# Kernel optimization log

Hardware: AMD Instinct MI355X
Metric: run time of the kernel (lower is better)

## Reference

```python
import jax, jax.numpy as jnp
import numpy as np

EPS = 1e-12  # matches torch F.normalize default eps

def l2norm(t):
    n = jnp.linalg.norm(t, axis=-1, keepdims=True)
    return t / jnp.maximum(n, EPS)

def rotate_half(x):
    # '... (j d) -> ... j d' with j=2: split into two halves, return cat(-x2, x1)
    x1, x2 = jnp.split(x, 2, axis=-1)
    return jnp.concatenate((-x2, x1), axis=-1)

def rotary_freqs(seq_len, dim):
    inv_freq = 1.0 / (10000.0 ** (jnp.arange(0, dim, 2, dtype=jnp.float32) / dim))
    seq = jnp.arange(seq_len, dtype=jnp.float32)
    freqs = seq[:, None] * inv_freq[None, :]          # [n, d/2]
    emb = jnp.concatenate((freqs, freqs), axis=-1)    # [n, d]
    return emb[None, None]                            # [1, 1, n, d]

def apply_rotary_pos_emb(t, freqs):
    # rot_dim == dim_head here, so the pass-through slice is empty
    return t * jnp.cos(freqs) + rotate_half(t) * jnp.sin(freqs)

def setup_inputs() -> dict:
    key = jax.random.key(0)
    kq, kk, kv = jax.random.split(key, 3)
    b, h, n, d = 2, 16, 2048, 64
    q = jax.random.normal(kq, (b, h, n, d), dtype=jnp.float32)
    k = jax.random.normal(kk, (b, h, n, d), dtype=jnp.float32)
    v = jax.random.normal(kv, (b, h, n, d), dtype=jnp.float32)
    q_scale = jnp.ones((d,), dtype=jnp.float32)
    k_scale = jnp.ones((d,), dtype=jnp.float32)
    return {"q": q, "k": k, "v": v, "q_scale": q_scale, "k_scale": k_scale}

def reference(q, k, v, q_scale, k_scale):
    b, h, n, d = q.shape
    # QK RMSNorm (l2 normalize + learned per-dim scale)
    q = l2norm(q) * q_scale
    k = l2norm(k) * k_scale
    # rotary position embedding (always applied in the source module)
    freqs = rotary_freqs(n, d)
    q = apply_rotary_pos_emb(q, freqs)
    k = apply_rotary_pos_emb(k, freqs)
    # attention: explicit scores -> softmax -> values
    scale = d ** -0.5
    sim = jnp.einsum('bhid,bhjd->bhij', q, k) * scale
    attn = jax.nn.softmax(sim, axis=-1)
    out = jnp.einsum('bhij,bhjd->bhid', attn, v)
    # 'b h n d -> b n (h d)'
    return out.transpose(0, 2, 1, 3).reshape(b, n, h * d)
```

## Files before the change

### kernel.cpp

```cpp
#include <hip/hip_runtime.h>
#include <math.h>

#define BH   32
#define NSEQ 2048
#define DH   64
#define NH   16
#define LOG2E 1.44269504088896f

typedef _Float16 f16x8 __attribute__((ext_vector_type(8)));
typedef __fp16   fp16x2 __attribute__((ext_vector_type(2)));
typedef float    f32x16v __attribute__((ext_vector_type(16)));

#if __has_builtin(__builtin_amdgcn_exp2f)
#define EXP2F(x) __builtin_amdgcn_exp2f(x)
#else
#define EXP2F(x) exp2f(x)
#endif

static __device__ __forceinline__ unsigned packh_rne(float a, float b) {
    union { _Float16 h[2]; unsigned u; } x;
    x.h[0] = (_Float16)a; x.h[1] = (_Float16)b;
    return x.u;
}
static __device__ __forceinline__ unsigned pkrtz(float a, float b) {
    fp16x2 r = __builtin_amdgcn_cvt_pkrtz(a, b);
    return __builtin_bit_cast(unsigned, r);
}
#if __has_builtin(__builtin_amdgcn_perm)
#define PERM(a, b, s) __builtin_amdgcn_perm((a), (b), (s))
#else
static __device__ __forceinline__ unsigned PERM(unsigned a, unsigned b, unsigned s) {
    if (s == 0x05040100u) return (b & 0xffffu) | (a << 16);
    return (b >> 16) | (a & 0xffff0000u);
}
#endif

static __device__ __forceinline__ void unpack_pairs(const unsigned* rr, uint4& lo, uint4& hi) {
    lo.x = PERM(rr[1], rr[0], 0x05040100u);  hi.x = PERM(rr[1], rr[0], 0x07060302u);
    lo.y = PERM(rr[3], rr[2], 0x05040100u);  hi.y = PERM(rr[3], rr[2], 0x07060302u);
    lo.z = PERM(rr[5], rr[4], 0x05040100u);  hi.z = PERM(rr[5], rr[4], 0x07060302u);
    lo.w = PERM(rr[7], rr[6], 0x05040100u);  hi.w = PERM(rr[7], rr[6], 0x07060302u);
}

__global__ void freq_kernel(float2* __restrict__ tab) {
    int idx = blockIdx.x * 256 + threadIdx.x;
    int pos = idx >> 5, p = idx & 31;
    float inv_freq = powf(10000.0f, -(float)p / 32.0f);
    float sn, cs;
    sincosf((float)pos * inv_freq, &sn, &cs);
    tab[idx] = make_float2(cs, sn);
}

__global__ void prep_kernel(const float* __restrict__ in, const float* __restrict__ scale,
                            const float2* __restrict__ tab,
                            unsigned* __restrict__ out, float smul) {
    const int w = threadIdx.x >> 6, lane = threadIdx.x & 63;
    const int c = lane & 31, hfr = lane >> 5;
    const int row = blockIdx.x * 8 + w * 2 + hfr;
    const size_t base = (size_t)row * DH;
    float2 x2 = *(const float2*)(in + base + 2 * c);
    float ss = x2.x * x2.x + x2.y * x2.y;
    #pragma unroll
    for (int off = 16; off > 0; off >>= 1) ss += __shfl_xor(ss, off);
    float inv = 1.0f / fmaxf(sqrtf(ss), 1e-12f);
    float2 sc = *(const float2*)(scale + 2 * c);
    float t0 = x2.x * inv * sc.x;
    float t1 = x2.y * inv * sc.y;
    float p0 = __shfl_xor(t0, 16);
    float p1 = __shfl_xor(t1, 16);
    float r0 = (c < 16) ? -p0 : p0;
    float r1 = (c < 16) ? -p1 : p1;
    int pos = row & (NSEQ - 1);
    float4 cc = *(const float4*)((const float*)(tab + pos * 32) + ((2 * c) & 31) * 2);
    float o0 = (t0 * cc.x + r0 * cc.y) * smul;
    float o1 = (t1 * cc.z + r1 * cc.w) * smul;
    out[row * 32 + c] = packh_rne(o0, o1);
}

__global__ void vpack_kernel(const float* __restrict__ v, unsigned* __restrict__ vt2) {
    const int kt = blockIdx.x, bh = blockIdx.y;
    const int t = threadIdx.x;
    const int r = t & 63, ch = t >> 6;
    const float* src = v + ((size_t)bh * NSEQ + kt * 64 + r) * DH + ch * 16;
    float4 a = *(const float4*)(src + 0);
    float4 b = *(const float4*)(src + 4);
    float4 c2 = *(const float4*)(src + 8);
    float4 d2 = *(const float4*)(src + 12);
    unsigned* dst = vt2 + ((size_t)bh * 32 + ch * 8) * NSEQ + kt * 64 + r;
    dst[0 * NSEQ] = packh_rne(a.x, a.y);
    dst[1 * NSEQ] = packh_rne(a.z, a.w);
    dst[2 * NSEQ] = packh_rne(b.x, b.y);
    dst[3 * NSEQ] = packh_rne(b.z, b.w);
    dst[4 * NSEQ] = packh_rne(c2.x, c2.y);
    dst[5 * NSEQ] = packh_rne(c2.z, c2.w);
    dst[6 * NSEQ] = packh_rne(d2.x, d2.y);
    dst[7 * NSEQ] = packh_rne(d2.z, d2.w);
}

__global__ __launch_bounds__(256, 2) void attn_kernel(
    const unsigned* __restrict__ qh, const unsigned* __restrict__ kh,
    const unsigned* __restrict__ vt2, float* __restrict__ out) {

    __shared__ _Float16 Ks[2][64 * 72];
    __shared__ _Float16 Vs[2][64 * 72];

    const int bh = blockIdx.y, qb = blockIdx.x;
    const int tid = threadIdx.x;
    const int w = tid >> 6, lane = tid & 63;
    const int c = lane & 31, hf = lane >> 5;

    const _Float16* qbase = (const _Float16*)qh + ((size_t)bh * NSEQ + qb * 128) * DH;
    const _Float16* kbase = (const _Float16*)kh + (size_t)bh * NSEQ * DH;
    const unsigned* vbase = vt2 + (size_t)bh * 32 * NSEQ;

    const int sdp = tid >> 3, skc = tid & 7;

    #pragma unroll
    for (int i = 0; i < 2; ++i) {
        int chunk = tid + 256 * i;
        int r = chunk >> 3, sg = chunk & 7;
        *(uint4*)&Ks[0][r * 72 + sg * 8] = *(const uint4*)(kbase + r * 64 + sg * 8);
    }
    {
        const unsigned* vsrc = vbase + (size_t)sdp * NSEQ + skc * 8;
        unsigned rr[8];
        #pragma unroll
        for (int j = 0; j < 8; ++j) rr[j] = vsrc[j];
        uint4 lo, hi;
        unpack_pairs(rr, lo, hi);
        *(uint4*)&Vs[0][(2 * sdp) * 72 + skc * 8]     = lo;
        *(uint4*)&Vs[0][(2 * sdp + 1) * 72 + skc * 8] = hi;
    }

    f16x8 qf[4];
    #pragma unroll
    for (int ks = 0; ks < 4; ++ks)
        qf[ks] = *(const f16x8*)(qbase + (w * 32 + c) * 64 + ks * 16 + hf * 8);

    f32x16v o[2];
    #pragma unroll
    for (int mt = 0; mt < 2; ++mt)
        #pragma unroll
        for (int r = 0; r < 16; ++r) o[mt][r] = 0.f;
    float lpart = 0.f;

    __syncthreads();

    for (int jt = 0; jt < 32; ++jt) {
        const int cur = jt & 1;
        uint4 kpre[2];
        unsigned vpre[8];
        if (jt + 1 < 32) {
            const _Float16* kn = kbase + (size_t)(jt + 1) * 64 * DH;
            #pragma unroll
            for (int i = 0; i < 2; ++i) {
                int chunk = tid + 256 * i;
                int r = chunk >> 3, sg = chunk & 7;
                kpre[i] = *(const uint4*)(kn + r * 64 + sg * 8);
            }
            const unsigned* vsrc = vbase + (size_t)sdp * NSEQ + (jt + 1) * 64 + skc * 8;
            #pragma unroll
            for (int j = 0; j < 8; ++j) vpre[j] = vsrc[j];
        }

        f32x16v s[2];
        #pragma unroll
        for (int mt = 0; mt < 2; ++mt)
            #pragma unroll
            for (int r = 0; r < 16; ++r) s[mt][r] = 0.f;
        #pragma unroll
        for (int ks = 0; ks < 4; ++ks) {
            f16x8 ka0 = *(const f16x8*)&Ks[cur][c * 72 + ks * 16 + hf * 8];
            f16x8 ka1 = *(const f16x8*)&Ks[cur][(32 + c) * 72 + ks * 16 + hf * 8];
            s[0] = __builtin_amdgcn_mfma_f32_32x32x16_f16(ka0, qf[ks], s[0], 0, 0, 0);
            s[1] = __builtin_amdgcn_mfma_f32_32x32x16_f16(ka1, qf[ks], s[1], 0, 0, 0);
        }

        #pragma unroll
        for (int mt = 0; mt < 2; ++mt)
            #pragma unroll
            for (int r = 0; r < 16; ++r) {
                float pv = EXP2F(s[mt][r]);
                s[mt][r] = pv;
                lpart += pv;
            }

        #pragma unroll
        for (int mt = 0; mt < 2; ++mt) {
            #pragma unroll
            for (int kk = 0; kk < 2; ++kk) {
                unsigned P01 = pkrtz(s[mt][kk * 8 + 0], s[mt][kk * 8 + 1]);
                unsigned P23 = pkrtz(s[mt][kk * 8 + 2], s[mt][kk * 8 + 3]);
                unsigned P45 = pkrtz(s[mt][kk * 8 + 4], s[mt][kk * 8 + 5]);
                unsigned P67 = pkrtz(s[mt][kk * 8 + 6], s[mt][kk * 8 + 7]);
                unsigned x01 = (unsigned)__shfl_xor((int)P01, 32);
                unsigned x23 = (unsigned)__shfl_xor((int)P23, 32);
                unsigned x45 = (unsigned)__shfl_xor((int)P45, 32);
                unsigned x67 = (unsigned)__shfl_xor((int)P67, 32);
                union { unsigned u[4]; f16x8 v; } B;
                B.u[0] = hf ? x45 : P01;
                B.u[1] = hf ? x67 : P23;
                B.u[2] = hf ? P45 : x01;
                B.u[3] = hf ? P67 : x23;
                const int kc = mt * 2 + kk;
                f16x8 va0 = *(const f16x8*)&Vs[cur][c * 72 + kc * 16 + hf * 8];
                f16x8 va1 = *(const f16x8*)&Vs[cur][(32 + c) * 72 + kc * 16 + hf * 8];
                o[0] = __builtin_amdgcn_mfma_f32_32x32x16_f16(va0, B.v, o[0], 0, 0, 0);
                o[1] = __builtin_amdgcn_mfma_f32_32x32x16_f16(va1, B.v, o[1], 0, 0, 0);
            }
        }

        if (jt + 1 < 32) {
            #pragma unroll
            for (int i = 0; i < 2; ++i) {
                int chunk = tid + 256 * i;
                int r = chunk >> 3, sg = chunk & 7;
                *(uint4*)&Ks[1 - cur][r * 72 + sg * 8] = kpre[i];
            }
            uint4 lo, hi;
            unpack_pairs(vpre, lo, hi);
            *(uint4*)&Vs[1 - cur][(2 * sdp) * 72 + skc * 8]     = lo;
            *(uint4*)&Vs[1 - cur][(2 * sdp + 1) * 72 + skc * 8] = hi;
        }
        __syncthreads();
    }

    float ltot = lpart + __shfl_xor(lpart, 32);
    float invl = 1.0f / ltot;
    const int b = bh >> 4, h = bh & 15;
    const int pos = qb * 128 + w * 32 + c;
    float* obase = out + ((size_t)b * NSEQ + pos) * (NH * DH) + h * DH;
    #pragma unroll
    for (int mt = 0; mt < 2; ++mt)
        #pragma unroll
        for (int g = 0; g < 4; ++g) {
            float4 r4 = make_float4(o[mt][g * 4 + 0] * invl, o[mt][g * 4 + 1] * invl,
                                    o[mt][g * 4 + 2] * invl, o[mt][g * 4 + 3] * invl);
            *(float4*)(obase + mt * 32 + g * 8 + hf * 4) = r4;
        }
}

extern "C" void kernel_launch(void* const* d_in, const int* in_sizes, int n_in,
                              void* d_out, int out_size, void* d_ws, size_t ws_size,
                              hipStream_t stream) {
    const float* q  = (const float*)d_in[0];
    const float* k  = (const float*)d_in[1];
    const float* v  = (const float*)d_in[2];
    const float* qs = (const float*)d_in[3];
    const float* ks = (const float*)d_in[4];
    float* outp = (float*)d_out;

    unsigned* qh  = (unsigned*)d_ws;
    unsigned* kh  = qh + (size_t)BH * NSEQ * 32;
    unsigned* vt2 = kh + (size_t)BH * NSEQ * 32;
    float2*   tab = (float2*)(vt2 + (size_t)BH * NSEQ * 32);

    freq_kernel<<<256, 256, 0, stream>>>(tab);
    prep_kernel<<<BH * NSEQ / 8, 256, 0, stream>>>(q, qs, tab, qh, 0.125f * LOG2E);
    prep_kernel<<<BH * NSEQ / 8, 256, 0, stream>>>(k, ks, tab, kh, 1.0f);
    vpack_kernel<<<dim3(NSEQ / 64, BH), 256, 0, stream>>>(v, vt2);
    attn_kernel<<<dim3(NSEQ / 128, BH), 256, 0, stream>>>(qh, kh, vt2, outp);
}
```

Baseline: 154.1 us.

## Fuse prep kernels and split attention key range across two warp groups

Merges the frequency table, Q/K normalization+rotary and V packing into a single prep kernel, with sin/cos computed per block in shared memory. The attention kernel now uses 512 threads, where two groups of four waves each handle half of the key sequence with 32-key tiles, and partial outputs and row sums are combined through shared memory at the end. This is meant to cut launch overhead and raise per-block parallelism and occupancy. The cost is an extra shared-memory reduction, recomputed sincos per block, and smaller tiles with more barriers.

```diff
diff --git a/kernel.cpp b/kernel.cpp
--- a/kernel.cpp
+++ b/kernel.cpp
@@ -35,107 +35,109 @@
 }
 #endif
 
-static __device__ __forceinline__ void unpack_pairs(const unsigned* rr, uint4& lo, uint4& hi) {
-    lo.x = PERM(rr[1], rr[0], 0x05040100u);  hi.x = PERM(rr[1], rr[0], 0x07060302u);
-    lo.y = PERM(rr[3], rr[2], 0x05040100u);  hi.y = PERM(rr[3], rr[2], 0x07060302u);
-    lo.z = PERM(rr[5], rr[4], 0x05040100u);  hi.z = PERM(rr[5], rr[4], 0x07060302u);
-    lo.w = PERM(rr[7], rr[6], 0x05040100u);  hi.w = PERM(rr[7], rr[6], 0x07060302u);
-}
-
-__global__ void freq_kernel(float2* __restrict__ tab) {
-    int idx = blockIdx.x * 256 + threadIdx.x;
-    int pos = idx >> 5, p = idx & 31;
-    float inv_freq = powf(10000.0f, -(float)p / 32.0f);
-    float sn, cs;
-    sincosf((float)pos * inv_freq, &sn, &cs);
-    tab[idx] = make_float2(cs, sn);
-}
-
-__global__ void prep_kernel(const float* __restrict__ in, const float* __restrict__ scale,
-                            const float2* __restrict__ tab,
-                            unsigned* __restrict__ out, float smul) {
-    const int w = threadIdx.x >> 6, lane = threadIdx.x & 63;
-    const int c = lane & 31, hfr = lane >> 5;
-    const int row = blockIdx.x * 8 + w * 2 + hfr;
-    const size_t base = (size_t)row * DH;
-    float2 x2 = *(const float2*)(in + base + 2 * c);
-    float ss = x2.x * x2.x + x2.y * x2.y;
-    #pragma unroll
-    for (int off = 16; off > 0; off >>= 1) ss += __shfl_xor(ss, off);
-    float inv = 1.0f / fmaxf(sqrtf(ss), 1e-12f);
-    float2 sc = *(const float2*)(scale + 2 * c);
-    float t0 = x2.x * inv * sc.x;
-    float t1 = x2.y * inv * sc.y;
-    float p0 = __shfl_xor(t0, 16);
-    float p1 = __shfl_xor(t1, 16);
-    float r0 = (c < 16) ? -p0 : p0;
-    float r1 = (c < 16) ? -p1 : p1;
-    int pos = row & (NSEQ - 1);
-    float4 cc = *(const float4*)((const float*)(tab + pos * 32) + ((2 * c) & 31) * 2);
-    float o0 = (t0 * cc.x + r0 * cc.y) * smul;
-    float o1 = (t1 * cc.z + r1 * cc.w) * smul;
-    out[row * 32 + c] = packh_rne(o0, o1);
-}
-
-__global__ void vpack_kernel(const float* __restrict__ v, unsigned* __restrict__ vt2) {
-    const int kt = blockIdx.x, bh = blockIdx.y;
+__global__ __launch_bounds__(256) void prep_all(
+    const float* __restrict__ q, const float* __restrict__ k, const float* __restrict__ v,
+    const float* __restrict__ qs, const float* __restrict__ ksc,
+    unsigned* __restrict__ qh, unsigned* __restrict__ kh, unsigned* __restrict__ vt2) {
+    const int bid = blockIdx.x;
     const int t = threadIdx.x;
-    const int r = t & 63, ch = t >> 6;
-    const float* src = v + ((size_t)bh * NSEQ + kt * 64 + r) * DH + ch * 16;
-    float4 a = *(const float4*)(src + 0);
-    float4 b = *(const float4*)(src + 4);
-    float4 c2 = *(const float4*)(src + 8);
-    float4 d2 = *(const float4*)(src + 12);
-    unsigned* dst = vt2 + ((size_t)bh * 32 + ch * 8) * NSEQ + kt * 64 + r;
-    dst[0 * NSEQ] = packh_rne(a.x, a.y);
-    dst[1 * NSEQ] = packh_rne(a.z, a.w);
-    dst[2 * NSEQ] = packh_rne(b.x, b.y);
-    dst[3 * NSEQ] = packh_rne(b.z, b.w);
-    dst[4 * NSEQ] = packh_rne(c2.x, c2.y);
-    dst[5 * NSEQ] = packh_rne(c2.z, c2.w);
-    dst[6 * NSEQ] = packh_rne(d2.x, d2.y);
-    dst[7 * NSEQ] = packh_rne(d2.z, d2.w);
-}
-
-__global__ __launch_bounds__(256, 2) void attn_kernel(
-    const unsigned* __restrict__ qh, const unsigned* __restrict__ kh,
+    if (bid < 16384) {
+        const bool isq = bid < 8192;
+        const float* in = isq ? q : k;
+        const float* sc = isq ? qs : ksc;
+        unsigned* outp  = isq ? qh : kh;
+        const float smul = isq ? 0.125f * LOG2E : 1.0f;
+        const int sb = bid & 8191;
+        __shared__ float2 tab[8][32];
+        {
+            int pr = t >> 5, p = t & 31;
+            int pos = (sb * 8 + pr) & (NSEQ - 1);
+            float infr = exp2f(-(float)p * (13.287712379549449f / 32.0f));
+            float sn, cs;
+            sincosf((float)pos * infr, &sn, &cs);
+            tab[pr][p] = make_float2(cs, sn);
+        }
+        __syncthreads();
+        const int w = t >> 6, lane = t & 63;
+        const int c = lane & 31, hfr = lane >> 5;
+        const int rl = w * 2 + hfr;
+        const int row = sb * 8 + rl;
+        float2 x2 = *(const float2*)(in + (size_t)row * DH + 2 * c);
+        float ss = x2.x * x2.x + x2.y * x2.y;
+        #pragma unroll
+        for (int off = 16; off > 0; off >>= 1) ss += __shfl_xor(ss, off);
+        float inv = 1.0f / fmaxf(sqrtf(ss), 1e-12f);
+        float2 s2 = *(const float2*)(sc + 2 * c);
+        float t0 = x2.x * inv * s2.x;
+        float t1 = x2.y * inv * s2.y;
+        float p0 = __shfl_xor(t0, 16);
+        float p1 = __shfl_xor(t1, 16);
+        float r0 = (c < 16) ? -p0 : p0;
+        float r1 = (c < 16) ? -p1 : p1;
+        float4 cc = *(const float4*)&tab[rl][(2 * c) & 31];
+        float o0 = (t0 * cc.x + r0 * cc.y) * smul;
+        float o1 = (t1 * cc.z + r1 * cc.w) * smul;
+        outp[row * 32 + c] = packh_rne(o0, o1);
+    } else {
+        const int sb = bid - 16384;
+        const int kt = sb & 31, bh = sb >> 5;
+        const int r = t & 63, ch = t >> 6;
+        const float* src = v + ((size_t)bh * NSEQ + kt * 64 + r) * DH + ch * 16;
+        float4 a = *(const float4*)(src + 0);
+        float4 b = *(const float4*)(src + 4);
+        float4 c2 = *(const float4*)(src + 8);
+        float4 d2 = *(const float4*)(src + 12);
+        unsigned* dst = vt2 + ((size_t)bh * 32 + ch * 8) * NSEQ + kt * 64 + r;
+        dst[0 * NSEQ] = packh_rne(a.x, a.y);
+        dst[1 * NSEQ] = packh_rne(a.z, a.w);
+        dst[2 * NSEQ] = packh_rne(b.x, b.y);
+        dst[3 * NSEQ] = packh_rne(b.z, b.w);
+        dst[4 * NSEQ] = packh_rne(c2.x, c2.y);
+        dst[5 * NSEQ] = packh_rne(c2.z, c2.w);
+        dst[6 * NSEQ] = packh_rne(d2.x, d2.y);
+        dst[7 * NSEQ] = packh_rne(d2.z, d2.w);
+    }
+}
+
+__global__ __launch_bounds__(512, 4) void attn_kernel(
+    const unsigned* __restrict__ qh, const unsigned* __restrict__ khg,
     const unsigned* __restrict__ vt2, float* __restrict__ out) {
 
-    __shared__ _Float16 Ks[2][64 * 72];
-    __shared__ _Float16 Vs[2][64 * 72];
+    __shared__ __align__(16) unsigned char SMEM[36864];
+    _Float16* KsB = (_Float16*)SMEM;
+    _Float16* VsB = (_Float16*)(SMEM + 18432);
+    float* Red = (float*)SMEM;
 
     const int bh = blockIdx.y, qb = blockIdx.x;
     const int tid = threadIdx.x;
-    const int w = tid >> 6, lane = tid & 63;
+    const int kh = tid >> 8;
+    const int ltid = tid & 255;
+    const int w = tid >> 6, wq = w & 3;
+    const int lane = tid & 63;
     const int c = lane & 31, hf = lane >> 5;
 
     const _Float16* qbase = (const _Float16*)qh + ((size_t)bh * NSEQ + qb * 128) * DH;
-    const _Float16* kbase = (const _Float16*)kh + (size_t)bh * NSEQ * DH;
-    const unsigned* vbase = vt2 + (size_t)bh * 32 * NSEQ;
-
-    const int sdp = tid >> 3, skc = tid & 7;
-
-    #pragma unroll
-    for (int i = 0; i < 2; ++i) {
-        int chunk = tid + 256 * i;
-        int r = chunk >> 3, sg = chunk & 7;
-        *(uint4*)&Ks[0][r * 72 + sg * 8] = *(const uint4*)(kbase + r * 64 + sg * 8);
-    }
+    const _Float16* kbase = (const _Float16*)khg + ((size_t)bh * NSEQ + kh * 1024) * DH;
+    const unsigned* vbase = vt2 + (size_t)bh * 32 * NSEQ + kh * 1024;
+
+    const int skr = ltid >> 3, ssg = ltid & 7;
+    const int sdp = ltid >> 3, skq = (ltid & 7) * 4;
+
     {
-        const unsigned* vsrc = vbase + (size_t)sdp * NSEQ + skc * 8;
-        unsigned rr[8];
-        #pragma unroll
-        for (int j = 0; j < 8; ++j) rr[j] = vsrc[j];
-        uint4 lo, hi;
-        unpack_pairs(rr, lo, hi);
-        *(uint4*)&Vs[0][(2 * sdp) * 72 + skc * 8]     = lo;
-        *(uint4*)&Vs[0][(2 * sdp + 1) * 72 + skc * 8] = hi;
+        *(uint4*)&KsB[(kh * 2 + 0) * 2304 + skr * 72 + ssg * 8] =
+            *(const uint4*)(kbase + skr * DH + ssg * 8);
+        uint4 vr = *(const uint4*)(vbase + (size_t)sdp * NSEQ + skq);
+        uint2 lo, hi;
+        lo.x = PERM(vr.y, vr.x, 0x05040100u); hi.x = PERM(vr.y, vr.x, 0x07060302u);
+        lo.y = PERM(vr.w, vr.z, 0x05040100u); hi.y = PERM(vr.w, vr.z, 0x07060302u);
+        *(uint2*)&VsB[(kh * 2 + 0) * 2304 + (2 * sdp) * 36 + skq]     = lo;
+        *(uint2*)&VsB[(kh * 2 + 0) * 2304 + (2 * sdp + 1) * 36 + skq] = hi;
     }
 
     f16x8 qf[4];
     #pragma unroll
     for (int ks = 0; ks < 4; ++ks)
-        qf[ks] = *(const f16x8*)(qbase + (w * 32 + c) * 64 + ks * 16 + hf * 8);
+        qf[ks] = *(const f16x8*)(qbase + (wq * 32 + c) * DH + ks * 16 + hf * 8);
 
     f32x16v o[2];
     #pragma unroll
@@ -148,96 +150,96 @@
 
     for (int jt = 0; jt < 32; ++jt) {
         const int cur = jt & 1;
-        uint4 kpre[2];
-        unsigned vpre[8];
+        const _Float16* KsCur = KsB + (kh * 2 + cur) * 2304;
+        const _Float16* VsCur = VsB + (kh * 2 + cur) * 2304;
+
+        uint4 kpre, vpre;
         if (jt + 1 < 32) {
-            const _Float16* kn = kbase + (size_t)(jt + 1) * 64 * DH;
-            #pragma unroll
-            for (int i = 0; i < 2; ++i) {
-                int chunk = tid + 256 * i;
-                int r = chunk >> 3, sg = chunk & 7;
-                kpre[i] = *(const uint4*)(kn + r * 64 + sg * 8);
-            }
-            const unsigned* vsrc = vbase + (size_t)sdp * NSEQ + (jt + 1) * 64 + skc * 8;
-            #pragma unroll
-            for (int j = 0; j < 8; ++j) vpre[j] = vsrc[j];
-        }
-
-        f32x16v s[2];
+            kpre = *(const uint4*)(kbase + (size_t)(jt + 1) * 32 * DH + skr * DH + ssg * 8);
+            vpre = *(const uint4*)(vbase + (size_t)sdp * NSEQ + (jt + 1) * 32 + skq);
+        }
+
+        f32x16v s;
+        #pragma unroll
+        for (int r = 0; r < 16; ++r) s[r] = 0.f;
+        #pragma unroll
+        for (int ks = 0; ks < 4; ++ks) {
+            f16x8 ka = *(const f16x8*)&KsCur[c * 72 + ks * 16 + hf * 8];
+            s = __builtin_amdgcn_mfma_f32_32x32x16_f16(ka, qf[ks], s, 0, 0, 0);
+        }
+
+        #pragma unroll
+        for (int r = 0; r < 16; ++r) {
+            float pv = EXP2F(s[r]);
+            s[r] = pv;
+            lpart += pv;
+        }
+
+        #pragma unroll
+        for (int kk = 0; kk < 2; ++kk) {
+            unsigned P01 = pkrtz(s[kk * 8 + 0], s[kk * 8 + 1]);
+            unsigned P23 = pkrtz(s[kk * 8 + 2], s[kk * 8 + 3]);
+            unsigned P45 = pkrtz(s[kk * 8 + 4], s[kk * 8 + 5]);
+            unsigned P67 = pkrtz(s[kk * 8 + 6], s[kk * 8 + 7]);
+            unsigned x01 = (unsigned)__shfl_xor((int)P01, 32);
+            unsigned x23 = (unsigned)__shfl_xor((int)P23, 32);
+            unsigned x45 = (unsigned)__shfl_xor((int)P45, 32);
+            unsigned x67 = (unsigned)__shfl_xor((int)P67, 32);
+            union { unsigned u[4]; f16x8 v; } B;
+            B.u[0] = hf ? x45 : P01;
+            B.u[1] = hf ? x67 : P23;
+            B.u[2] = hf ? P45 : x01;
+            B.u[3] = hf ? P67 : x23;
+            f16x8 va0 = *(const f16x8*)&VsCur[c * 36 + kk * 16 + hf * 8];
+            f16x8 va1 = *(const f16x8*)&VsCur[(32 + c) * 36 + kk * 16 + hf * 8];
+            o[0] = __builtin_amdgcn_mfma_f32_32x32x16_f16(va0, B.v, o[0], 0, 0, 0);
+            o[1] = __builtin_amdgcn_mfma_f32_32x32x16_f16(va1, B.v, o[1], 0, 0, 0);
+        }
+
+        if (jt + 1 < 32) {
+            _Float16* KsN = KsB + (kh * 2 + (1 - cur)) * 2304;
+            _Float16* VsN = VsB + (kh * 2 + (1 - cur)) * 2304;
+            *(uint4*)&KsN[skr * 72 + ssg * 8] = kpre;
+            uint2 lo, hi;
+            lo.x = PERM(kpre.y, kpre.x, 0u);
+            lo.x = PERM(vpre.y, vpre.x, 0x05040100u); hi.x = PERM(vpre.y, vpre.x, 0x07060302u);
+            lo.y = PERM(vpre.w, vpre.z, 0x05040100u); hi.y = PERM(vpre.w, vpre.z, 0x07060302u);
+            *(uint2*)&VsN[(2 * sdp) * 36 + skq]     = lo;
+            *(uint2*)&VsN[(2 * sdp + 1) * 36 + skq] = hi;
+        }
+        __syncthreads();
+    }
+
+    if (kh == 1) {
+        float* r = Red + ((size_t)wq * 64 + lane) * 33;
+        #pragma unroll
+        for (int i = 0; i < 16; ++i) r[i] = o[0][i];
+        #pragma unroll
+        for (int i = 0; i < 16; ++i) r[16 + i] = o[1][i];
+        r[32] = lpart;
+    }
+    __syncthreads();
+    if (kh == 0) {
+        const float* r = Red + ((size_t)wq * 64 + lane) * 33;
+        #pragma unroll
+        for (int i = 0; i < 16; ++i) o[0][i] += r[i];
+        #pragma unroll
+        for (int i = 0; i < 16; ++i) o[1][i] += r[16 + i];
+        lpart += r[32];
+        float ltot = lpart + __shfl_xor(lpart, 32);
+        float invl = 1.0f / ltot;
+        const int b = bh >> 4, h = bh & 15;
+        const int pos = qb * 128 + wq * 32 + c;
+        float* obase = out + ((size_t)b * NSEQ + pos) * (NH * DH) + h * DH;
         #pragma unroll
         for (int mt = 0; mt < 2; ++mt)
             #pragma unroll
-            for (int r = 0; r < 16; ++r) s[mt][r] = 0.f;
-        #pragma unroll
-        for (int ks = 0; ks < 4; ++ks) {
-            f16x8 ka0 = *(const f16x8*)&Ks[cur][c * 72 + ks * 16 + hf * 8];
-            f16x8 ka1 = *(const f16x8*)&Ks[cur][(32 + c) * 72 + ks * 16 + hf * 8];
-            s[0] = __builtin_amdgcn_mfma_f32_32x32x16_f16(ka0, qf[ks], s[0], 0, 0, 0);
-            s[1] = __builtin_amdgcn_mfma_f32_32x32x16_f16(ka1, qf[ks], s[1], 0, 0, 0);
-        }
-
-        #pragma unroll
-        for (int mt = 0; mt < 2; ++mt)
-            #pragma unroll
-            for (int r = 0; r < 16; ++r) {
-                float pv = EXP2F(s[mt][r]);
-                s[mt][r] = pv;
-                lpart += pv;
+            for (int g = 0; g < 4; ++g) {
+                float4 r4 = make_float4(o[mt][g * 4 + 0] * invl, o[mt][g * 4 + 1] * invl,
+                                        o[mt][g * 4 + 2] * invl, o[mt][g * 4 + 3] * invl);
+                *(float4*)(obase + mt * 32 + g * 8 + hf * 4) = r4;
             }
-
-        #pragma unroll
-        for (int mt = 0; mt < 2; ++mt) {
-            #pragma unroll
-            for (int kk = 0; kk < 2; ++kk) {
-                unsigned P01 = pkrtz(s[mt][kk * 8 + 0], s[mt][kk * 8 + 1]);
-                unsigned P23 = pkrtz(s[mt][kk * 8 + 2], s[mt][kk * 8 + 3]);
-                unsigned P45 = pkrtz(s[mt][kk * 8 + 4], s[mt][kk * 8 + 5]);
-                unsigned P67 = pkrtz(s[mt][kk * 8 + 6], s[mt][kk * 8 + 7]);
-                unsigned x01 = (unsigned)__shfl_xor((int)P01, 32);
-                unsigned x23 = (unsigned)__shfl_xor((int)P23, 32);
-                unsigned x45 = (unsigned)__shfl_xor((int)P45, 32);
-                unsigned x67 = (unsigned)__shfl_xor((int)P67, 32);
-                union { unsigned u[4]; f16x8 v; } B;
-                B.u[0] = hf ? x45 : P01;
-                B.u[1] = hf ? x67 : P23;
-                B.u[2] = hf ? P45 : x01;
-                B.u[3] = hf ? P67 : x23;
-                const int kc = mt * 2 + kk;
-                f16x8 va0 = *(const f16x8*)&Vs[cur][c * 72 + kc * 16 + hf * 8];
-                f16x8 va1 = *(const f16x8*)&Vs[cur][(32 + c) * 72 + kc * 16 + hf * 8];
-                o[0] = __builtin_amdgcn_mfma_f32_32x32x16_f16(va0, B.v, o[0], 0, 0, 0);
-                o[1] = __builtin_amdgcn_mfma_f32_32x32x16_f16(va1, B.v, o[1], 0, 0, 0);
-            }
-        }
-
-        if (jt + 1 < 32) {
-            #pragma unroll
-            for (int i = 0; i < 2; ++i) {
-                int chunk = tid + 256 * i;
-                int r = chunk >> 3, sg = chunk & 7;
-                *(uint4*)&Ks[1 - cur][r * 72 + sg * 8] = kpre[i];
-            }
-            uint4 lo, hi;
-            unpack_pairs(vpre, lo, hi);
-            *(uint4*)&Vs[1 - cur][(2 * sdp) * 72 + skc * 8]     = lo;
-            *(uint4*)&Vs[1 - cur][(2 * sdp + 1) * 72 + skc * 8] = hi;
-        }
-        __syncthreads();
-    }
-
-    float ltot = lpart + __shfl_xor(lpart, 32);
-    float invl = 1.0f / ltot;
-    const int b = bh >> 4, h = bh & 15;
-    const int pos = qb * 128 + w * 32 + c;
-    float* obase = out + ((size_t)b * NSEQ + pos) * (NH * DH) + h * DH;
-    #pragma unroll
-    for (int mt = 0; mt < 2; ++mt)
-        #pragma unroll
-        for (int g = 0; g < 4; ++g) {
-            float4 r4 = make_float4(o[mt][g * 4 + 0] * invl, o[mt][g * 4 + 1] * invl,
-                                    o[mt][g * 4 + 2] * invl, o[mt][g * 4 + 3] * invl);
-            *(float4*)(obase + mt * 32 + g * 8 + hf * 4) = r4;
-        }
+    }
 }
 
 extern "C" void kernel_launch(void* const* d_in, const int* in_sizes, int n_in,
@@ -253,11 +255,7 @@
     unsigned* qh  = (unsigned*)d_ws;
     unsigned* kh  = qh + (size_t)BH * NSEQ * 32;
     unsigned* vt2 = kh + (size_t)BH * NSEQ * 32;
-    float2*   tab = (float2*)(vt2 + (size_t)BH * NSEQ * 32);
-
-    freq_kernel<<<256, 256, 0, stream>>>(tab);
-    prep_kernel<<<BH * NSEQ / 8, 256, 0, stream>>>(q, qs, tab, qh, 0.125f * LOG2E);
-    prep_kernel<<<BH * NSEQ / 8, 256, 0, stream>>>(k, ks, tab, kh, 1.0f);
-    vpack_kernel<<<dim3(NSEQ / 64, BH), 256, 0, stream>>>(v, vt2);
-    attn_kernel<<<dim3(NSEQ / 128, BH), 256, 0, stream>>>(qh, kh, vt2, outp);
-}
+
+    prep_all<<<17408, 256, 0, stream>>>(q, k, v, qs, ks, qh, kh, vt2);
+    attn_kernel<<<dim3(NSEQ / 128, BH), 512, 0, stream>>>(qh, kh, vt2, outp);
+}
```

Result: slower. 189.6 us (+23.0%).
